# Optimization experiments

Hardware: AMD Instinct MI355X
Metric: run time of the kernel (lower is better)

Reference implementation:

```python
import jax, jax.numpy as jnp
import numpy as np

N_GRAPHS = 256
BN_EPS = 1e-5

def gcn_conv(x, row, col, W, b, n):
    # PyG GCNConv: add self-loops, symmetric deg^-1/2 normalization, scatter-add at col.
    deg = jnp.zeros((n,), x.dtype).at[col].add(1.0) + 1.0  # +1 for self-loop
    dinv = jax.lax.rsqrt(deg)
    xw = x @ W                                             # [N, H]
    msg = (dinv[row] * dinv[col])[:, None] * xw[row]       # [E, H] gathered messages
    agg = jnp.zeros_like(xw).at[col].add(msg)              # scatter-add to targets
    agg = agg + (dinv * dinv)[:, None] * xw                # self-loop contribution
    return agg + b

def batch_norm(x, gamma, beta):
    # BatchNorm1d over the node dimension (training-mode batch statistics)
    mu = jnp.mean(x, axis=0)
    var = jnp.var(x, axis=0)
    return (x - mu) * jax.lax.rsqrt(var + BN_EPS) * gamma + beta

def setup_inputs():
    key = jax.random.key(0)
    ks = jax.random.split(key, 8)
    N, F, H, C, E = 50000, 128, 128, 3, 1_600_000
    x = jax.random.normal(ks[0], (N, F), jnp.float32)
    edge_index = jax.random.randint(ks[1], (2, E), 0, N)
    batch = jnp.sort(jax.random.randint(ks[2], (N,), 0, N_GRAPHS))
    s = lambda k, sh, fan: jax.random.normal(k, sh, jnp.float32) / np.sqrt(fan).astype(np.float32)
    return {
        "x": x, "edge_index": edge_index, "batch": batch,
        "W1": s(ks[3], (F, H), F), "b1": jnp.zeros((H,), jnp.float32),
        "gamma1": jnp.ones((H,), jnp.float32), "beta1": jnp.zeros((H,), jnp.float32),
        "W2": s(ks[4], (H, H), H), "b2": jnp.zeros((H,), jnp.float32),
        "gamma2": jnp.ones((H,), jnp.float32), "beta2": jnp.zeros((H,), jnp.float32),
        "Wc": s(ks[5], (3 * H, C), 3 * H), "bc": jnp.zeros((C,), jnp.float32),
    }

def reference(x, edge_index, batch, W1, b1, gamma1, beta1, W2, b2, gamma2, beta2, Wc, bc):
    n = x.shape[0]
    row, col = edge_index[0], edge_index[1]
    h = jax.nn.relu(batch_norm(gcn_conv(x, row, col, W1, b1, n), gamma1, beta1))
    # dropout is identity in eval mode
    h = jax.nn.relu(batch_norm(gcn_conv(h, row, col, W2, b2, n), gamma2, beta2))
    cnt = jax.ops.segment_sum(jnp.ones((n,), h.dtype), batch, num_segments=N_GRAPHS)
    hsum = jax.ops.segment_sum(h, batch, num_segments=N_GRAPHS)
    hmean = hsum / jnp.maximum(cnt, 1.0)[:, None]
    hmax = jax.ops.segment_max(h, batch, num_segments=N_GRAPHS)
    hmax = jnp.where(cnt[:, None] > 0, hmax, 0.0)  # guard empty graphs
    g = jnp.concatenate([hmean, hmax, hsum], axis=1)  # [G, 3H]
    return g @ Wc + bc
```

## Files before the change

### kernel.cpp

```cpp
#include <hip/hip_runtime.h>

#define HF 128
#define TILE 128
#define CAP2 6144
#define NFINE_MAX 512
#define SORT_CHUNK 4096
#define BN_EPS 1e-5f
#define SMEM_BYTES 34816

__device__ __forceinline__ unsigned short f2bf(float f) {
    unsigned u = __float_as_uint(f);
    unsigned rounding = 0x7FFF + ((u >> 16) & 1);
    return (unsigned short)((u + rounding) >> 16);
}
__device__ __forceinline__ float bf2f(unsigned short u) {
    return __uint_as_float(((unsigned)u) << 16);
}
__device__ __forceinline__ unsigned packbf(float lo, float hi) {
    return ((unsigned)f2bf(hi) << 16) | (unsigned)f2bf(lo);
}

__device__ __forceinline__ void bucket_sort_block(char* smem, int bid,
                                                  const int* __restrict__ row,
                                                  const int* __restrict__ col,
                                                  unsigned* __restrict__ buckets,
                                                  int* __restrict__ cursor,
                                                  int E, int nfine) {
    unsigned* staged = (unsigned*)smem;
    unsigned short* sbkt = (unsigned short*)(smem + 16384);
    int* hist  = (int*)(smem + 24576);
    int* lbase = (int*)(smem + 26624);
    int* gbase = (int*)(smem + 28672);
    int* lofs  = (int*)(smem + 30720);
    int* s     = (int*)(smem + 32768);
    int t = threadIdx.x;
    for (int i = t; i < NFINE_MAX; i += 256) { hist[i] = 0; lofs[i] = 0; }
    __syncthreads();
    int e0 = bid * SORT_CHUNK;
    int n = min(SORT_CHUNK, E - e0);
    for (int i = t; i < n; i += 256) {
        int c = col[e0 + i];
        atomicAdd(&hist[c >> 7], 1);
    }
    __syncthreads();
    s[t] = hist[t];
    s[t + 256] = hist[t + 256];
    for (int o = 1; o < 512; o <<= 1) {
        __syncthreads();
        int idx = (t + 1) * (o << 1) - 1;
        if (idx < 512) s[idx] += s[idx - o];
    }
    __syncthreads();
    if (t == 0) s[511] = 0;
    for (int o = 256; o >= 1; o >>= 1) {
        __syncthreads();
        int idx = (t + 1) * (o << 1) - 1;
        if (idx < 512) { int tmp = s[idx - o]; s[idx - o] = s[idx]; s[idx] += tmp; }
    }
    __syncthreads();
    lbase[t] = s[t];
    lbase[t + 256] = s[t + 256];
    for (int b = t; b < nfine; b += 256) {
        int cnt = hist[b];
        gbase[b] = cnt ? atomicAdd(&cursor[b * 16], cnt) : 0;
    }
    __syncthreads();
    for (int i = t; i < n; i += 256) {
        int c = col[e0 + i];
        int r = row[e0 + i];
        int b = c >> 7;
        int pos = lbase[b] + atomicAdd(&lofs[b], 1);
        staged[pos] = ((unsigned)(c & 127) << 17) | (unsigned)r;
        sbkt[pos] = (unsigned short)b;
    }
    __syncthreads();
    for (int i = t; i < n; i += 256) {
        int b = sbkt[i];
        int pos = gbase[b] + (i - lbase[b]);
        if (pos < CAP2) buckets[(size_t)b * CAP2 + pos] = staged[i];
    }
}

__device__ __forceinline__ void gemm_block(char* smem, int bid,
                                           const float* __restrict__ Xf,
                                           const unsigned short* __restrict__ Xh,
                                           const float* __restrict__ W,
                                           unsigned short* __restrict__ Y,
                                           const float* __restrict__ scale,
                                           const float* __restrict__ shift,
                                           const float* __restrict__ rowscale,
                                           int N, int applyBN) {
    float (*xst)[68] = (float(*)[68])smem;
    int t = threadIdx.x;
    int row0 = bid * 64;
    {
        int f = t & 127;
        float sc = applyBN ? scale[f] : 1.0f;
        float sh = applyBN ? shift[f] : 0.0f;
        for (int r = (t >> 7); r < 64; r += 2) {
            int rr = row0 + r;
            float v = 0.0f;
            if (rr < N) {
                if (applyBN) {
                    v = bf2f(Xh[(size_t)rr * HF + f]);
                    v = fmaxf(v * sc + sh, 0.0f);
                } else {
                    v = Xf[(size_t)rr * HF + f];
                }
            }
            xst[f][r] = v;
        }
    }
    __syncthreads();
    int cg = t & 31;
    int rg = t >> 5;
    int r0 = rg * 8;
    float acc[8][4] = {};
    const float4* Wv = reinterpret_cast<const float4*>(W);
    #pragma unroll 2
    for (int f = 0; f < HF; ++f) {
        float4 w = Wv[f * 32 + cg];
        float4 x0 = *reinterpret_cast<const float4*>(&xst[f][r0]);
        float4 x1 = *reinterpret_cast<const float4*>(&xst[f][r0 + 4]);
        float xr[8] = {x0.x, x0.y, x0.z, x0.w, x1.x, x1.y, x1.z, x1.w};
        #pragma unroll
        for (int i = 0; i < 8; ++i) {
            acc[i][0] += xr[i] * w.x;
            acc[i][1] += xr[i] * w.y;
            acc[i][2] += xr[i] * w.z;
            acc[i][3] += xr[i] * w.w;
        }
    }
    #pragma unroll
    for (int i = 0; i < 8; ++i) {
        int rr = row0 + r0 + i;
        if (rr < N) {
            float rs = rowscale ? rowscale[rr] : 1.0f;
            ushort4 o;
            o.x = f2bf(acc[i][0] * rs);
            o.y = f2bf(acc[i][1] * rs);
            o.z = f2bf(acc[i][2] * rs);
            o.w = f2bf(acc[i][3] * rs);
            *reinterpret_cast<ushort4*>(&Y[(size_t)rr * HF + cg * 4]) = o;
        }
    }
}

__global__ __launch_bounds__(256) void sort_gemm1(const int* __restrict__ row,
                                                  const int* __restrict__ col,
                                                  unsigned* __restrict__ buckets,
                                                  int* __restrict__ cursor,
                                                  int E, int nfine, int nsort,
                                                  const float* __restrict__ x,
                                                  const float* __restrict__ W1,
                                                  unsigned short* __restrict__ A,
                                                  int N) {
    __shared__ __align__(16) char smem[SMEM_BYTES];
    if (blockIdx.x < nsort)
        bucket_sort_block(smem, blockIdx.x, row, col, buckets, cursor, E, nfine);
    else
        gemm_block(smem, blockIdx.x - nsort, x, nullptr, W1, A,
                   nullptr, nullptr, nullptr, N, 0);
}

__global__ __launch_bounds__(256) void gemm_rt(const unsigned short* __restrict__ Xh,
                                               const float* __restrict__ W,
                                               unsigned short* __restrict__ Y,
                                               const float* __restrict__ scale,
                                               const float* __restrict__ shift,
                                               const float* __restrict__ rowscale,
                                               int N) {
    __shared__ __align__(16) char smem[SMEM_BYTES];
    gemm_block(smem, blockIdx.x, nullptr, Xh, W, Y, scale, shift, rowscale, N, 1);
}

__global__ __launch_bounds__(256) void scale_rows(unsigned short* __restrict__ A,
                                                  const float* __restrict__ dinv,
                                                  int N) {
    int idx = blockIdx.x * 256 + threadIdx.x;
    int n = idx >> 4, j = idx & 15;
    if (n >= N) return;
    float dc = dinv[n];
    const unsigned M = 0xffff0000u;
    uint4 u = *reinterpret_cast<const uint4*>(A + (size_t)n * HF + j * 8);
    uint4 o;
    o.x = packbf(__uint_as_float(u.x << 16) * dc, __uint_as_float(u.x & M) * dc);
    o.y = packbf(__uint_as_float(u.y << 16) * dc, __uint_as_float(u.y & M) * dc);
    o.z = packbf(__uint_as_float(u.z << 16) * dc, __uint_as_float(u.z & M) * dc);
    o.w = packbf(__uint_as_float(u.w << 16) * dc, __uint_as_float(u.w & M) * dc);
    *reinterpret_cast<uint4*>(A + (size_t)n * HF + j * 8) = o;
}

__global__ __launch_bounds__(256) void tile_place2(const unsigned* __restrict__ buckets,
                                                   const int* __restrict__ cursor,
                                                   int* __restrict__ rowptr,
                                                   float* __restrict__ dinv,
                                                   int* __restrict__ srow,
                                                   const int* __restrict__ batch,
                                                   int* __restrict__ gstart,
                                                   int N, int NG, int nfine) {
    int b = blockIdx.x;
    int t = threadIdx.x;
    if (b < 2 && t < 129) {
        int g = b * 129 + t;
        if (g <= NG) {
            int lo = 0, hi = N;
            while (lo < hi) {
                int mid = (lo + hi) >> 1;
                if (batch[mid] < g) lo = mid + 1; else hi = mid;
            }
            gstart[g] = lo;
        }
    }
    __shared__ int h[TILE], loc[TILE], cur[TILE];
    __shared__ int red[256];
    __shared__ int stage[CAP2];
    int part = 0;
    for (int i = t; i < b; i += 256) part += min(cursor[i * 16], CAP2);
    red[t] = part;
    if (t < TILE) h[t] = 0;
    __syncthreads();
    for (int o = 128; o > 0; o >>= 1) {
        if (t < o) red[t] += red[t + o];
        __syncthreads();
    }
    int base = red[0];
    int sz = min(cursor[b * 16], CAP2);
    const unsigned* bk = buckets + (size_t)b * CAP2;
    for (int i = t; i < sz; i += 256) atomicAdd(&h[bk[i] >> 17], 1);
    __syncthreads();
    if (t < TILE) loc[t] = h[t];
    __syncthreads();
    for (int o = 1; o < TILE; o <<= 1) {
        int v = (t < TILE && t >= o) ? loc[t - o] : 0;
        __syncthreads();
        if (t < TILE) loc[t] += v;
        __syncthreads();
    }
    if (t < TILE) {
        int c = b * TILE + t;
        int excl = loc[t] - h[t];
        if (c < N) {
            rowptr[c] = base + excl;
            dinv[c] = rsqrtf((float)h[t] + 1.0f);
        }
        cur[t] = excl;
    }
    if (b == nfine - 1 && t == 0) rowptr[N] = base + sz;
    __syncthreads();
    for (int i = t; i < sz; i += 256) {
        unsigned p = bk[i];
        int pos = atomicAdd(&cur[p >> 17], 1);
        if (pos < CAP2) stage[pos] = (int)(p & 0x1FFFFu);
    }
    __syncthreads();
    for (int i = t; i < sz; i += 256) srow[base + i] = stage[i];
}

__global__ __launch_bounds__(256) void gather_conv(const int* __restrict__ rowptr,
                                                   const int* __restrict__ srow,
                                                   const float* __restrict__ dinv,
                                                   const unsigned short* __restrict__ XW,
                                                   const float* __restrict__ b,
                                                   unsigned short* __restrict__ OUT,
                                                   float* __restrict__ psum,
                                                   float* __restrict__ psq, int N) {
    int blk = blockIdx.x;
    int c = blk * 16 + (threadIdx.x >> 4);
    int j = threadIdx.x & 15;
    bool valid = (c < N);
    const unsigned M = 0xffff0000u;
    float o[8];
    if (valid) {
        int e = rowptr[c], end = rowptr[c + 1];
        float acc[8] = {0.f, 0.f, 0.f, 0.f, 0.f, 0.f, 0.f, 0.f};
        for (; e + 3 < end; e += 4) {
            int r0 = srow[e], r1 = srow[e + 1], r2 = srow[e + 2], r3 = srow[e + 3];
            uint4 u0 = *reinterpret_cast<const uint4*>(XW + (size_t)r0 * HF + j * 8);
            uint4 u1 = *reinterpret_cast<const uint4*>(XW + (size_t)r1 * HF + j * 8);
            uint4 u2 = *reinterpret_cast<const uint4*>(XW + (size_t)r2 * HF + j * 8);
            uint4 u3 = *reinterpret_cast<const uint4*>(XW + (size_t)r3 * HF + j * 8);
            acc[0] += (__uint_as_float(u0.x << 16) + __uint_as_float(u1.x << 16))
                    + (__uint_as_float(u2.x << 16) + __uint_as_float(u3.x << 16));
            acc[1] += (__uint_as_float(u0.x & M) + __uint_as_float(u1.x & M))
                    + (__uint_as_float(u2.x & M) + __uint_as_float(u3.x & M));
            acc[2] += (__uint_as_float(u0.y << 16) + __uint_as_float(u1.y << 16))
                    + (__uint_as_float(u2.y << 16) + __uint_as_float(u3.y << 16));
            acc[3] += (__uint_as_float(u0.y & M) + __uint_as_float(u1.y & M))
                    + (__uint_as_float(u2.y & M) + __uint_as_float(u3.y & M));
            acc[4] += (__uint_as_float(u0.z << 16) + __uint_as_float(u1.z << 16))
                    + (__uint_as_float(u2.z << 16) + __uint_as_float(u3.z << 16));
            acc[5] += (__uint_as_float(u0.z & M) + __uint_as_float(u1.z & M))
                    + (__uint_as_float(u2.z & M) + __uint_as_float(u3.z & M));
            acc[6] += (__uint_as_float(u0.w << 16) + __uint_as_float(u1.w << 16))
                    + (__uint_as_float(u2.w << 16) + __uint_as_float(u3.w << 16));
            acc[7] += (__uint_as_float(u0.w & M) + __uint_as_float(u1.w & M))
                    + (__uint_as_float(u2.w & M) + __uint_as_float(u3.w & M));
        }
        for (; e < end; ++e) {
            int r0 = srow[e];
            uint4 u0 = *reinterpret_cast<const uint4*>(XW + (size_t)r0 * HF + j * 8);
            acc[0] += __uint_as_float(u0.x << 16);
            acc[1] += __uint_as_float(u0.x & M);
            acc[2] += __uint_as_float(u0.y << 16);
            acc[3] += __uint_as_float(u0.y & M);
            acc[4] += __uint_as_float(u0.z << 16);
            acc[5] += __uint_as_float(u0.z & M);
            acc[6] += __uint_as_float(u0.w << 16);
            acc[7] += __uint_as_float(u0.w & M);
        }
        float dc = dinv[c];
        uint4 xv = *reinterpret_cast<const uint4*>(XW + (size_t)c * HF + j * 8);
        acc[0] += __uint_as_float(xv.x << 16);
        acc[1] += __uint_as_float(xv.x & M);
        acc[2] += __uint_as_float(xv.y << 16);
        acc[3] += __uint_as_float(xv.y & M);
        acc[4] += __uint_as_float(xv.z << 16);
        acc[5] += __uint_as_float(xv.z & M);
        acc[6] += __uint_as_float(xv.w << 16);
        acc[7] += __uint_as_float(xv.w & M);
        float4 b0 = *reinterpret_cast<const float4*>(b + j * 8);
        float4 b1 = *reinterpret_cast<const float4*>(b + j * 8 + 4);
        o[0] = dc * acc[0] + b0.x;
        o[1] = dc * acc[1] + b0.y;
        o[2] = dc * acc[2] + b0.z;
        o[3] = dc * acc[3] + b0.w;
        o[4] = dc * acc[4] + b1.x;
        o[5] = dc * acc[5] + b1.y;
        o[6] = dc * acc[6] + b1.z;
        o[7] = dc * acc[7] + b1.w;
        uint4 ov;
        ov.x = packbf(o[0], o[1]);
        ov.y = packbf(o[2], o[3]);
        ov.z = packbf(o[4], o[5]);
        ov.w = packbf(o[6], o[7]);
        *reinterpret_cast<uint4*>(OUT + (size_t)c * HF + j * 8) = ov;
    } else {
        #pragma unroll
        for (int k = 0; k < 8; ++k) o[k] = 0.f;
    }
    __shared__ float sval[16][HF + 4];
    int r = threadIdx.x >> 4;
    *reinterpret_cast<float4*>(&sval[r][j * 8]) = make_float4(o[0], o[1], o[2], o[3]);
    *reinterpret_cast<float4*>(&sval[r][j * 8 + 4]) = make_float4(o[4], o[5], o[6], o[7]);
    __syncthreads();
    if (threadIdx.x < HF) {
        float s = 0.f, sq = 0.f;
        #pragma unroll
        for (int rr = 0; rr < 16; ++rr) {
            float v = sval[rr][threadIdx.x];
            s += v;
            sq += v * v;
        }
        psum[(size_t)blk * HF + threadIdx.x] = s;
        psq[(size_t)blk * HF + threadIdx.x] = sq;
    }
}

__global__ __launch_bounds__(256) void bn_reduce(const float* __restrict__ psum,
                                                 const float* __restrict__ psq,
                                                 const float* __restrict__ gamma,
                                                 const float* __restrict__ beta,
                                                 float* __restrict__ scale,
                                                 float* __restrict__ shift,
                                                 int nblk, int N) {
    int f = blockIdx.x;
    int t = threadIdx.x;
    float s = 0.f, sq = 0.f;
    for (int i = t; i < nblk; i += 256) {
        s += psum[(size_t)i * HF + f];
        sq += psq[(size_t)i * HF + f];
    }
    __shared__ float ls[256], lq[256];
    ls[t] = s; lq[t] = sq;
    __syncthreads();
    for (int o = 128; o > 0; o >>= 1) {
        if (t < o) { ls[t] += ls[t + o]; lq[t] += lq[t + o]; }
        __syncthreads();
    }
    if (t == 0) {
        float invn = 1.0f / (float)N;
        float mu = ls[0] * invn;
        float var = lq[0] * invn - mu * mu;
        float sc = gamma[f] * rsqrtf(var + BN_EPS);
        scale[f] = sc;
        shift[f] = beta[f] - mu * sc;
    }
}

__global__ __launch_bounds__(256) void pool_classify(const unsigned short* __restrict__ Bh,
                                                     const int* __restrict__ gstart,
                                                     const float* __restrict__ scale,
                                                     const float* __restrict__ shift,
                                                     const float* __restrict__ Wc,
                                                     const float* __restrict__ bc,
                                                     float* __restrict__ out) {
    int g = blockIdx.x;
    int t = threadIdx.x & 127;
    int half = threadIdx.x >> 7;
    int s0 = gstart[g], s1 = gstart[g + 1];
    float sc = scale[t], sh = shift[t];
    float sum = 0.f, mx = 0.f;
    for (int n = s0 + half; n < s1; n += 2) {
        float v = fmaxf(bf2f(Bh[(size_t)n * HF + t]) * sc + sh, 0.0f);
        sum += v;
        mx = fmaxf(mx, v);
    }
    __shared__ float shsum[2][HF], shmax[2][HF];
    __shared__ float red[3][HF];
    shsum[half][t] = sum;
    shmax[half][t] = mx;
    __syncthreads();
    if (half == 0) {
        sum += shsum[1][t];
        mx = fmaxf(mx, shmax[1][t]);
        float cntf = (float)(s1 - s0);
        float mean = sum / fmaxf(cntf, 1.0f);
        red[0][t] = mean * Wc[t * 3 + 0] + mx * Wc[(HF + t) * 3 + 0] + sum * Wc[(2 * HF + t) * 3 + 0];
        red[1][t] = mean * Wc[t * 3 + 1] + mx * Wc[(HF + t) * 3 + 1] + sum * Wc[(2 * HF + t) * 3 + 1];
        red[2][t] = mean * Wc[t * 3 + 2] + mx * Wc[(HF + t) * 3 + 2] + sum * Wc[(2 * HF + t) * 3 + 2];
    }
    __syncthreads();
    for (int o = 64; o > 0; o >>= 1) {
        if (half == 0 && t < o) {
            red[0][t] += red[0][t + o];
            red[1][t] += red[1][t + o];
            red[2][t] += red[2][t + o];
        }
        __syncthreads();
    }
    if (threadIdx.x < 3) out[g * 3 + threadIdx.x] = red[threadIdx.x][0] + bc[threadIdx.x];
}

extern "C" void kernel_launch(void* const* d_in, const int* in_sizes, int n_in,
                              void* d_out, int out_size, void* d_ws, size_t ws_size,
                              hipStream_t stream) {
    const float* x    = (const float*)d_in[0];
    const int*   ei   = (const int*)d_in[1];
    const int*   batch= (const int*)d_in[2];
    const float* W1   = (const float*)d_in[3];
    const float* b1   = (const float*)d_in[4];
    const float* g1   = (const float*)d_in[5];
    const float* be1  = (const float*)d_in[6];
    const float* W2   = (const float*)d_in[7];
    const float* b2   = (const float*)d_in[8];
    const float* g2   = (const float*)d_in[9];
    const float* be2  = (const float*)d_in[10];
    const float* Wc   = (const float*)d_in[11];
    const float* bc   = (const float*)d_in[12];
    float* out = (float*)d_out;

    const int N = in_sizes[0] / HF;
    const int E = in_sizes[1] / 2;
    const int NG = 256;
    const int* row = ei;
    const int* col = ei + E;
    const int total = N * HF;
    const int nfine = (N + TILE - 1) / TILE;
    const int nblkGa = (N + 15) / 16;

    char* w = (char*)d_ws;
    size_t off = 0;
    auto alloc = [&](size_t bytes) -> void* {
        void* p = w + off;
        off += (bytes + 255) & ~(size_t)255;
        return p;
    };
    int*            cursor    = (int*)alloc((size_t)nfine * 16 * 4);
    float*          dinv      = (float*)alloc((size_t)N * 4);
    int*            rowptr    = (int*)alloc(((size_t)N + 1) * 4);
    int*            gstart    = (int*)alloc((NG + 1) * 4);
    int*            srow      = (int*)alloc((size_t)E * 4);
    float*          psum      = (float*)alloc((size_t)nblkGa * HF * 4);
    float*          psq       = (float*)alloc((size_t)nblkGa * HF * 4);
    float*          scale     = (float*)alloc(HF * 4);
    float*          shift     = (float*)alloc(HF * 4);
    unsigned short* A         = (unsigned short*)alloc((size_t)total * 2);
    unsigned short* B         = (unsigned short*)alloc((size_t)total * 2);
    unsigned*       buckets   = (unsigned*)B;

    const int T256 = 256;
    int gridGemm = (N + 63) / 64;
    int nsort    = (E + SORT_CHUNK - 1) / SORT_CHUNK;
    int gridScl  = (N * 16 + 255) / 256;

    hipMemsetAsync(cursor, 0, (size_t)nfine * 16 * 4, stream);
    sort_gemm1<<<nsort + gridGemm, T256, 0, stream>>>(row, col, buckets, cursor,
                                                      E, nfine, nsort, x, W1, A, N);
    tile_place2<<<nfine, T256, 0, stream>>>(buckets, cursor, rowptr, dinv, srow,
                                            batch, gstart, N, NG, nfine);
    scale_rows<<<gridScl, T256, 0, stream>>>(A, dinv, N);

    gather_conv<<<nblkGa, T256, 0, stream>>>(rowptr, srow, dinv, A, b1, B, psum, psq, N);
    bn_reduce<<<HF, 256, 0, stream>>>(psum, psq, g1, be1, scale, shift, nblkGa, N);

    gemm_rt<<<gridGemm, T256, 0, stream>>>(B, W2, A, scale, shift, dinv, N);
    gather_conv<<<nblkGa, T256, 0, stream>>>(rowptr, srow, dinv, A, b2, B, psum, psq, N);
    bn_reduce<<<HF, 256, 0, stream>>>(psum, psq, g2, be2, scale, shift, nblkGa, N);

    pool_classify<<<NG, 256, 0, stream>>>(B, gstart, scale, shift, Wc, bc, out);
}
```

Before: 282.2 us.

## Fuse row scaling into tile placement and shrink sort/gemm1 block footprint

Removes the separate scale_rows kernel by applying the dinv row scaling to the bf16 XW1 rows inside tile_place2, which already computes the degrees for each 128-column tile. The bucket sort now uses 2048-edge chunks and has each thread load 8 edges with vectorized int4 reads held in registers, so col is no longer read twice. The first GEMM switches to 32-row blocks with a smaller shared-memory footprint to raise occupancy of the fused sort+gemm kernel. In exchange there are twice as many sort blocks doing global cursor atomics, and tile_place2 has more work per block.

```diff
diff --git a/kernel.cpp b/kernel.cpp
--- a/kernel.cpp
+++ b/kernel.cpp
@@ -4,9 +4,9 @@
 #define TILE 128
 #define CAP2 6144
 #define NFINE_MAX 512
-#define SORT_CHUNK 4096
+#define SORT_CHUNK 2048
 #define BN_EPS 1e-5f
-#define SMEM_BYTES 34816
+#define SMEM_FUSED 22528
 
 __device__ __forceinline__ unsigned short f2bf(float f) {
     unsigned u = __float_as_uint(f);
@@ -27,20 +27,45 @@
                                                   int* __restrict__ cursor,
                                                   int E, int nfine) {
     unsigned* staged = (unsigned*)smem;
-    unsigned short* sbkt = (unsigned short*)(smem + 16384);
-    int* hist  = (int*)(smem + 24576);
-    int* lbase = (int*)(smem + 26624);
-    int* gbase = (int*)(smem + 28672);
-    int* lofs  = (int*)(smem + 30720);
-    int* s     = (int*)(smem + 32768);
+    unsigned short* sbkt = (unsigned short*)(smem + 8192);
+    int* hist  = (int*)(smem + 12288);
+    int* lbase = (int*)(smem + 14336);
+    int* gbase = (int*)(smem + 16384);
+    int* lofs  = (int*)(smem + 18432);
+    int* s     = (int*)(smem + 20480);
     int t = threadIdx.x;
     for (int i = t; i < NFINE_MAX; i += 256) { hist[i] = 0; lofs[i] = 0; }
     __syncthreads();
-    int e0 = bid * SORT_CHUNK;
-    int n = min(SORT_CHUNK, E - e0);
-    for (int i = t; i < n; i += 256) {
-        int c = col[e0 + i];
-        atomicAdd(&hist[c >> 7], 1);
+    int e0 = bid * SORT_CHUNK + t * 8;
+    int cc[8], rr[8], pg[8];
+    unsigned pk[8];
+    if (e0 + 8 <= E) {
+        int4 c0 = *reinterpret_cast<const int4*>(col + e0);
+        int4 c1 = *reinterpret_cast<const int4*>(col + e0 + 4);
+        int4 r0 = *reinterpret_cast<const int4*>(row + e0);
+        int4 r1 = *reinterpret_cast<const int4*>(row + e0 + 4);
+        cc[0]=c0.x; cc[1]=c0.y; cc[2]=c0.z; cc[3]=c0.w;
+        cc[4]=c1.x; cc[5]=c1.y; cc[6]=c1.z; cc[7]=c1.w;
+        rr[0]=r0.x; rr[1]=r0.y; rr[2]=r0.z; rr[3]=r0.w;
+        rr[4]=r1.x; rr[5]=r1.y; rr[6]=r1.z; rr[7]=r1.w;
+    } else {
+        #pragma unroll
+        for (int i = 0; i < 8; ++i) {
+            int e = e0 + i;
+            cc[i] = (e < E) ? col[e] : -1;
+            rr[i] = (e < E) ? row[e] : 0;
+        }
+    }
+    #pragma unroll
+    for (int i = 0; i < 8; ++i) {
+        if (cc[i] >= 0) {
+            int b = cc[i] >> 7;
+            pg[i] = b;
+            pk[i] = ((unsigned)(cc[i] & 127) << 17) | (unsigned)rr[i];
+            atomicAdd(&hist[b], 1);
+        } else {
+            pg[i] = -1;
+        }
     }
     __syncthreads();
     s[t] = hist[t];
@@ -65,15 +90,16 @@
         gbase[b] = cnt ? atomicAdd(&cursor[b * 16], cnt) : 0;
     }
     __syncthreads();
-    for (int i = t; i < n; i += 256) {
-        int c = col[e0 + i];
-        int r = row[e0 + i];
-        int b = c >> 7;
-        int pos = lbase[b] + atomicAdd(&lofs[b], 1);
-        staged[pos] = ((unsigned)(c & 127) << 17) | (unsigned)r;
-        sbkt[pos] = (unsigned short)b;
-    }
-    __syncthreads();
+    #pragma unroll
+    for (int i = 0; i < 8; ++i) {
+        if (pg[i] >= 0) {
+            int pos = lbase[pg[i]] + atomicAdd(&lofs[pg[i]], 1);
+            staged[pos] = pk[i];
+            sbkt[pos] = (unsigned short)pg[i];
+        }
+    }
+    __syncthreads();
+    int n = min(SORT_CHUNK, E - bid * SORT_CHUNK);
     for (int i = t; i < n; i += 256) {
         int b = sbkt[i];
         int pos = gbase[b] + (i - lbase[b]);
@@ -81,32 +107,89 @@
     }
 }
 
-__device__ __forceinline__ void gemm_block(char* smem, int bid,
-                                           const float* __restrict__ Xf,
-                                           const unsigned short* __restrict__ Xh,
-                                           const float* __restrict__ W,
-                                           unsigned short* __restrict__ Y,
-                                           const float* __restrict__ scale,
-                                           const float* __restrict__ shift,
-                                           const float* __restrict__ rowscale,
-                                           int N, int applyBN) {
-    float (*xst)[68] = (float(*)[68])smem;
+__device__ __forceinline__ void gemm_block32(char* smem, int bid,
+                                             const float* __restrict__ X,
+                                             const float* __restrict__ W,
+                                             unsigned short* __restrict__ Y, int N) {
+    float (*xst)[36] = (float(*)[36])smem;
     int t = threadIdx.x;
-    int row0 = bid * 64;
+    int row0 = bid * 32;
     {
         int f = t & 127;
-        float sc = applyBN ? scale[f] : 1.0f;
-        float sh = applyBN ? shift[f] : 0.0f;
+        for (int r = (t >> 7); r < 32; r += 2) {
+            int rr = row0 + r;
+            xst[f][r] = (rr < N) ? X[(size_t)rr * HF + f] : 0.0f;
+        }
+    }
+    __syncthreads();
+    int cg = t & 31;
+    int rg = t >> 5;
+    int r0 = rg * 4;
+    float acc[4][4] = {};
+    const float4* Wv = reinterpret_cast<const float4*>(W);
+    #pragma unroll 4
+    for (int f = 0; f < HF; ++f) {
+        float4 w = Wv[f * 32 + cg];
+        float4 xv = *reinterpret_cast<const float4*>(&xst[f][r0]);
+        float xr[4] = {xv.x, xv.y, xv.z, xv.w};
+        #pragma unroll
+        for (int i = 0; i < 4; ++i) {
+            acc[i][0] += xr[i] * w.x;
+            acc[i][1] += xr[i] * w.y;
+            acc[i][2] += xr[i] * w.z;
+            acc[i][3] += xr[i] * w.w;
+        }
+    }
+    #pragma unroll
+    for (int i = 0; i < 4; ++i) {
+        int rr = row0 + r0 + i;
+        if (rr < N) {
+            ushort4 o;
+            o.x = f2bf(acc[i][0]);
+            o.y = f2bf(acc[i][1]);
+            o.z = f2bf(acc[i][2]);
+            o.w = f2bf(acc[i][3]);
+            *reinterpret_cast<ushort4*>(&Y[(size_t)rr * HF + cg * 4]) = o;
+        }
+    }
+}
+
+__global__ __launch_bounds__(256) void sort_gemm1(const int* __restrict__ row,
+                                                  const int* __restrict__ col,
+                                                  unsigned* __restrict__ buckets,
+                                                  int* __restrict__ cursor,
+                                                  int E, int nfine, int nsort,
+                                                  const float* __restrict__ x,
+                                                  const float* __restrict__ W1,
+                                                  unsigned short* __restrict__ A,
+                                                  int N) {
+    __shared__ __align__(16) char smem[SMEM_FUSED];
+    if (blockIdx.x < nsort)
+        bucket_sort_block(smem, blockIdx.x, row, col, buckets, cursor, E, nfine);
+    else
+        gemm_block32(smem, blockIdx.x - nsort, x, W1, A, N);
+}
+
+__global__ __launch_bounds__(256) void gemm_rt(const unsigned short* __restrict__ Xh,
+                                               const float* __restrict__ W,
+                                               unsigned short* __restrict__ Y,
+                                               const float* __restrict__ scale,
+                                               const float* __restrict__ shift,
+                                               const float* __restrict__ rowscale,
+                                               int N) {
+    __shared__ float xst[HF][68];
+    int t = threadIdx.x;
+    int row0 = blockIdx.x * 64;
+    {
+        int f = t & 127;
+        float sc = scale[f];
+        float sh = shift[f];
         for (int r = (t >> 7); r < 64; r += 2) {
             int rr = row0 + r;
             float v = 0.0f;
             if (rr < N) {
-                if (applyBN) {
-                    v = bf2f(Xh[(size_t)rr * HF + f]);
-                    v = fmaxf(v * sc + sh, 0.0f);
-                } else {
-                    v = Xf[(size_t)rr * HF + f];
-                }
+                v = bf2f(Xh[(size_t)rr * HF + f]);
+                v = fmaxf(v * sc + sh, 0.0f);
             }
             xst[f][r] = v;
         }
@@ -135,7 +218,7 @@
     for (int i = 0; i < 8; ++i) {
         int rr = row0 + r0 + i;
         if (rr < N) {
-            float rs = rowscale ? rowscale[rr] : 1.0f;
+            float rs = rowscale[rr];
             ushort4 o;
             o.x = f2bf(acc[i][0] * rs);
             o.y = f2bf(acc[i][1] * rs);
@@ -146,56 +229,12 @@
     }
 }
 
-__global__ __launch_bounds__(256) void sort_gemm1(const int* __restrict__ row,
-                                                  const int* __restrict__ col,
-                                                  unsigned* __restrict__ buckets,
-                                                  int* __restrict__ cursor,
-                                                  int E, int nfine, int nsort,
-                                                  const float* __restrict__ x,
-                                                  const float* __restrict__ W1,
-                                                  unsigned short* __restrict__ A,
-                                                  int N) {
-    __shared__ __align__(16) char smem[SMEM_BYTES];
-    if (blockIdx.x < nsort)
-        bucket_sort_block(smem, blockIdx.x, row, col, buckets, cursor, E, nfine);
-    else
-        gemm_block(smem, blockIdx.x - nsort, x, nullptr, W1, A,
-                   nullptr, nullptr, nullptr, N, 0);
-}
-
-__global__ __launch_bounds__(256) void gemm_rt(const unsigned short* __restrict__ Xh,
-                                               const float* __restrict__ W,
-                                               unsigned short* __restrict__ Y,
-                                               const float* __restrict__ scale,
-                                               const float* __restrict__ shift,
-                                               const float* __restrict__ rowscale,
-                                               int N) {
-    __shared__ __align__(16) char smem[SMEM_BYTES];
-    gemm_block(smem, blockIdx.x, nullptr, Xh, W, Y, scale, shift, rowscale, N, 1);
-}
-
-__global__ __launch_bounds__(256) void scale_rows(unsigned short* __restrict__ A,
-                                                  const float* __restrict__ dinv,
-                                                  int N) {
-    int idx = blockIdx.x * 256 + threadIdx.x;
-    int n = idx >> 4, j = idx & 15;
-    if (n >= N) return;
-    float dc = dinv[n];
-    const unsigned M = 0xffff0000u;
-    uint4 u = *reinterpret_cast<const uint4*>(A + (size_t)n * HF + j * 8);
-    uint4 o;
-    o.x = packbf(__uint_as_float(u.x << 16) * dc, __uint_as_float(u.x & M) * dc);
-    o.y = packbf(__uint_as_float(u.y << 16) * dc, __uint_as_float(u.y & M) * dc);
-    o.z = packbf(__uint_as_float(u.z << 16) * dc, __uint_as_float(u.z & M) * dc);
-    o.w = packbf(__uint_as_float(u.w << 16) * dc, __uint_as_float(u.w & M) * dc);
-    *reinterpret_cast<uint4*>(A + (size_t)n * HF + j * 8) = o;
-}
-
 __global__ __launch_bounds__(256) void tile_place2(const unsigned* __restrict__ buckets,
                                                    const int* __restrict__ cursor,
                                                    int* __restrict__ rowptr,
                                                    float* __restrict__ dinv,
                                                    int* __restrict__ srow,
+                                                   unsigned short* __restrict__ A,
                                                    const int* __restrict__ batch,
                                                    int* __restrict__ gstart,
                                                    int N, int NG, int nfine) {
@@ -213,6 +252,7 @@
         }
     }
     __shared__ int h[TILE], loc[TILE], cur[TILE];
+    __shared__ float dloc[TILE];
     __shared__ int red[256];
     __shared__ int stage[CAP2];
     int part = 0;
@@ -237,13 +277,17 @@
         if (t < TILE) loc[t] += v;
         __syncthreads();
     }
+    int c0 = b * TILE;
+    int ncols = min(TILE, N - c0);
     if (t < TILE) {
-        int c = b * TILE + t;
+        int c = c0 + t;
         int excl = loc[t] - h[t];
+        float dc = rsqrtf((float)h[t] + 1.0f);
         if (c < N) {
             rowptr[c] = base + excl;
-            dinv[c] = rsqrtf((float)h[t] + 1.0f);
-        }
+            dinv[c] = dc;
+        }
+        dloc[t] = dc;
         cur[t] = excl;
     }
     if (b == nfine - 1 && t == 0) rowptr[N] = base + sz;
@@ -255,6 +299,19 @@
     }
     __syncthreads();
     for (int i = t; i < sz; i += 256) srow[base + i] = stage[i];
+    const unsigned M = 0xffff0000u;
+    for (int i = t; i < ncols * 16; i += 256) {
+        int nl = i >> 4, j = i & 15;
+        float dc = dloc[nl];
+        unsigned short* ap = A + (size_t)(c0 + nl) * HF + j * 8;
+        uint4 u = *reinterpret_cast<const uint4*>(ap);
+        uint4 o;
+        o.x = packbf(__uint_as_float(u.x << 16) * dc, __uint_as_float(u.x & M) * dc);
+        o.y = packbf(__uint_as_float(u.y << 16) * dc, __uint_as_float(u.y & M) * dc);
+        o.z = packbf(__uint_as_float(u.z << 16) * dc, __uint_as_float(u.z & M) * dc);
+        o.w = packbf(__uint_as_float(u.w << 16) * dc, __uint_as_float(u.w & M) * dc);
+        *reinterpret_cast<uint4*>(ap) = o;
+    }
 }
 
 __global__ __launch_bounds__(256) void gather_conv(const int* __restrict__ rowptr,
@@ -480,21 +537,20 @@
     unsigned*       buckets   = (unsigned*)B;
 
     const int T256 = 256;
-    int gridGemm = (N + 63) / 64;
-    int nsort    = (E + SORT_CHUNK - 1) / SORT_CHUNK;
-    int gridScl  = (N * 16 + 255) / 256;
+    int gridGemm64 = (N + 63) / 64;
+    int gridGemm32 = (N + 31) / 32;
+    int nsort      = (E + SORT_CHUNK - 1) / SORT_CHUNK;
 
     hipMemsetAsync(cursor, 0, (size_t)nfine * 16 * 4, stream);
-    sort_gemm1<<<nsort + gridGemm, T256, 0, stream>>>(row, col, buckets, cursor,
-                                                      E, nfine, nsort, x, W1, A, N);
-    tile_place2<<<nfine, T256, 0, stream>>>(buckets, cursor, rowptr, dinv, srow,
+    sort_gemm1<<<nsort + gridGemm32, T256, 0, stream>>>(row, col, buckets, cursor,
+                                                        E, nfine, nsort, x, W1, A, N);
+    tile_place2<<<nfine, T256, 0, stream>>>(buckets, cursor, rowptr, dinv, srow, A,
                                             batch, gstart, N, NG, nfine);
-    scale_rows<<<gridScl, T256, 0, stream>>>(A, dinv, N);
 
     gather_conv<<<nblkGa, T256, 0, stream>>>(rowptr, srow, dinv, A, b1, B, psum, psq, N);
     bn_reduce<<<HF, 256, 0, stream>>>(psum, psq, g1, be1, scale, shift, nblkGa, N);
 
-    gemm_rt<<<gridGemm, T256, 0, stream>>>(B, W2, A, scale, shift, dinv, N);
+    gemm_rt<<<gridGemm64, T256, 0, stream>>>(B, W2, A, scale, shift, dinv, N);
     gather_conv<<<nblkGa, T256, 0, stream>>>(rowptr, srow, dinv, A, b2, B, psum, psq, N);
     bn_reduce<<<HF, 256, 0, stream>>>(psum, psq, g2, be2, scale, shift, nblkGa, N);
 
```

New measurement: 292.8 us. +3.8%, slower.
